# Kernel tuning notes

Measured on AMD Instinct MI355X. Metric: run time of the kernel, lower is better.

The kernel has to match this reference:

```python
import jax, jax.numpy as jnp
import numpy as np

APREC = 8   # activation fractional bits
PPREC = 8   # parameter fractional bits
IWIDTH = 3  # integer width -> clamp to [-2**IWIDTH, 2**IWIDTH - 1]

QMAX = 2.0 ** IWIDTH - 1.0
QMIN = -(2.0 ** IWIDTH)


def quant(v, prec):
    # round to 2**-prec grid (torch.round and jnp.round both round-half-to-even)
    s = 2.0 ** prec
    return jnp.round(v * s) / s


def round_max(v):
    # the relu-chain in the source is exactly a clamp to [QMIN, QMAX]
    return jnp.clip(v, QMIN, QMAX)


def fixed_point_conv(x, w, b):
    """Quantized 'conv': each elementwise product w[j,m,p,q]*x[b,m,k+p,l+q] is
    rounded to the activation grid and clamped BEFORE summation, then bias added.
    x: [B,Cin,H,W], w: [Cout,Cin,K,K], b: [Cout].
    Loop is over the KxK fixed kernel offsets (25), fully vectorized over B/Cout/Cin/space."""
    w = quant(w, PPREC)
    b = quant(b, PPREC)
    K = w.shape[2]
    Ho = x.shape[2] - K + 1
    Wo = x.shape[3] - K + 1
    out = jnp.zeros((x.shape[0], w.shape[0], Ho, Wo), dtype=x.dtype)
    for p in range(K):
        for q in range(K):
            # [B, Cout, Cin, Ho, Wo]
            prod = x[:, None, :, p:p + Ho, q:q + Wo] * w[None, :, :, p, q, None, None]
            prod = round_max(quant(prod, APREC))
            out = out + prod.sum(axis=2)
    return out + b[None, :, None, None]


def fixed_point_fc(x, w, b):
    # x: [B, in], w: [out, in], b: [out]
    w = round_max(quant(w, PPREC))
    b = round_max(quant(b, PPREC))
    x = round_max(quant(x, APREC))
    out = x @ w.T + b[None, :]
    out = round_max(out)
    return quant(out, APREC)


def max_pool2(x):
    return jax.lax.reduce_window(x, -jnp.inf, jax.lax.max,
                                 (1, 1, 2, 2), (1, 1, 2, 2), 'VALID')


def setup_inputs() -> dict:
    key = jax.random.key(0)
    ks = jax.random.split(key, 9)
    B = 2048
    return {
        'x': jax.random.normal(ks[0], (B, 1, 28, 28), jnp.float32),
        'conv1_w': jax.random.normal(ks[1], (10, 1, 5, 5), jnp.float32) * 0.2,
        'conv1_b': jax.random.normal(ks[2], (10,), jnp.float32) * 0.1,
        'conv2_w': jax.random.normal(ks[3], (20, 10, 5, 5), jnp.float32) * 0.1,
        'conv2_b': jax.random.normal(ks[4], (20,), jnp.float32) * 0.1,
        'fc1_w': jax.random.normal(ks[5], (50, 320), jnp.float32) * 0.05,
        'fc1_b': jax.random.normal(ks[6], (50,), jnp.float32) * 0.05,
        'fc2_w': jax.random.normal(ks[7], (10, 50), jnp.float32) * 0.1,
        'fc2_b': jax.random.normal(ks[8], (10,), jnp.float32) * 0.1,
    }


def reference(x, conv1_w, conv1_b, conv2_w, conv2_b, fc1_w, fc1_b, fc2_w, fc2_b):
    x = quant(x, APREC)
    conv1_input = x
    x = fixed_point_conv(x, conv1_w, conv1_b)          # [B,10,24,24]
    x = quant(x, APREC)
    conv1_output = x
    x = jax.nn.relu(max_pool2(x))                      # [B,10,12,12]
    x = quant(x, APREC)
    conv2_input = x
    x = fixed_point_conv(x, conv2_w, conv2_b)          # [B,20,8,8]
    x = quant(x, APREC)
    conv2_output = x
    # Dropout2d / F.dropout are identity in eval mode
    x = jax.nn.relu(max_pool2(x))                      # [B,20,4,4]
    x = x.reshape(-1, 320)
    x = quant(x, APREC)
    fc1_input = x
    x = fixed_point_fc(x, fc1_w, fc1_b)                # [B,50]
    x = quant(x, APREC)
    fc1_output = x
    x = jax.nn.relu(x)
    x = quant(x, APREC)
    fc2_input = x
    x = fixed_point_fc(x, fc2_w, fc2_b)                # [B,10]
    x = quant(x, APREC)
    fc2_output = x
    logp = jax.nn.log_softmax(x, axis=1)
    return (logp, conv1_input, conv1_output, conv2_input, conv2_output,
            fc1_input, fc1_output, fc2_input, fc2_output)
```

## Files before the change

kernel.cpp:

```cpp
#include <hip/hip_runtime.h>
#include <math.h>


#define NB 2048

#define OFF_LOGP   0
#define OFF_C1IN   (OFF_LOGP  + NB*10)
#define OFF_C1OUT  (OFF_C1IN  + NB*784)
#define OFF_C2IN   (OFF_C1OUT + NB*5760)
#define OFF_C2OUT  (OFF_C2IN  + NB*1440)
#define OFF_FC1IN  (OFF_C2OUT + NB*1280)
#define OFF_FC1OUT (OFF_FC1IN + NB*320)
#define OFF_FC2IN  (OFF_FC1OUT+ NB*50)
#define OFF_FC2OUT (OFF_FC2IN + NB*50)

#define MAGIC_F 12582912.0f

#define WS_WT1 0
#define WS_B1  20480
#define WS_WT2 20544
#define WS_B2  21344

__device__ __forceinline__ float clamp8(float v) {
    return __builtin_amdgcn_fmed3f(v, -8.0f, 7.0f);
}

__global__ __launch_bounds__(512, 6)
void k12_convs(const float* __restrict__ x,
               const float* __restrict__ cw1, const float* __restrict__ cb1,
               const float* __restrict__ cw2, const float* __restrict__ cb2,
               const float* __restrict__ fw1, const float* __restrict__ fb1,
               const float* __restrict__ fw2, const float* __restrict__ fb2,
               float* __restrict__ ws,
               float* __restrict__ out)
{
    __shared__ __align__(16) float s_w1[280];
    __shared__ float s_b1[10];
    __shared__ __align__(16) float s_w2[5600];
    __shared__ float s_b2[20];
    __shared__ __align__(16) float s_x[784];
    __shared__ __align__(16) float s_p1[1440];

    const int t   = threadIdx.x;
    const int img = blockIdx.x;

    if (t < 250)                 s_w1[(t/25)*28 + (t%25)] = rintf(cw1[t] * 256.0f);
    else if (t >= 256 && t < 266) s_b1[t - 256] = rintf(cb1[t - 256] * 256.0f);
    else if (t >= 288 && t < 308) s_b2[t - 288] = rintf(cb2[t - 288] * 256.0f);
    for (int idx = t; idx < 5000; idx += 512) {
        int cc = idx / 25, q = idx % 25;
        s_w2[cc * 28 + q] = rintf(cw2[idx] * 256.0f);
    }
    const float* xg = x + (size_t)img * 784;
    float* c1in_g = out + OFF_C1IN + (size_t)img * 784;
    for (int i = t; i < 784; i += 512) {
        float v = rintf(xg[i] * 256.0f) * (1.0f / 256.0f);
        s_x[i] = v;
        c1in_g[i] = v;
    }
    __syncthreads();

    if (t < 480) {
        const int co = t / 48;
        const int r  = t % 48;
        const int i  = r >> 1;
        const int jh = r & 1;

        float wreg[28];
        {
            const float* wb = s_w1 + co * 28;
            #pragma unroll
            for (int k = 0; k < 7; k++) {
                float4 v4 = *(const float4*)(wb + 4 * k);
                wreg[4*k] = v4.x; wreg[4*k+1] = v4.y; wreg[4*k+2] = v4.z; wreg[4*k+3] = v4.w;
            }
        }

        float acc[12];
        #pragma unroll
        for (int j = 0; j < 12; j++) acc[j] = MAGIC_F;

        #pragma unroll
        for (int p = 0; p < 5; p++) {
            float xr[16];
            const float* row = &s_x[(i + p) * 28 + 12 * jh];
            #pragma unroll
            for (int k = 0; k < 4; k++) {
                float4 v4 = *(const float4*)(row + 4 * k);
                xr[4*k] = v4.x; xr[4*k+1] = v4.y; xr[4*k+2] = v4.z; xr[4*k+3] = v4.w;
            }
            #pragma unroll
            for (int q = 0; q < 5; q++) {
                float w = wreg[p * 5 + q];
                #pragma unroll
                for (int j = 0; j < 12; j++)
                    acc[j] = fmaf(xr[q + j], w, acc[j]);
            }
        }
        const float C = MAGIC_F - s_b1[co];
        float v[12];
        #pragma unroll
        for (int j = 0; j < 12; j++) v[j] = (acc[j] - C) * (1.0f / 256.0f);

        float* gdst = out + OFF_C1OUT + (size_t)img * 5760 + co * 576 + i * 24 + 12 * jh;
        #pragma unroll
        for (int k = 0; k < 3; k++) {
            float4 st = { v[4*k], v[4*k+1], v[4*k+2], v[4*k+3] };
            *(float4*)(gdst + 4 * k) = st;
        }

        float m[6];
        #pragma unroll
        for (int j2 = 0; j2 < 6; j2++) m[j2] = fmaxf(v[2*j2], v[2*j2+1]);
        float pm[6];
        #pragma unroll
        for (int j2 = 0; j2 < 6; j2++) pm[j2] = __shfl_xor(m[j2], 2);

        if ((i & 1) == 0) {
            float pr[6];
            #pragma unroll
            for (int j2 = 0; j2 < 6; j2++)
                pr[j2] = fmaxf(fmaxf(m[j2], pm[j2]), 0.0f);
            const int o = co * 144 + (i >> 1) * 12 + 6 * jh;
            float* g = out + OFF_C2IN + (size_t)img * 1440 + o;
            #pragma unroll
            for (int k = 0; k < 3; k++) {
                float2 st = { pr[2*k], pr[2*k+1] };
                *(float2*)(g + 2 * k) = st;
                s_p1[o + 2*k]     = pr[2*k];
                s_p1[o + 2*k + 1] = pr[2*k + 1];
            }
        }
    }
    __syncthreads();

    if (t < 320) {
        const int ch = t & 1;
        const int rc = t >> 1;
        const int co = rc >> 3;
        const int i  = rc & 7;

        float acc[8];
        #pragma unroll
        for (int j = 0; j < 8; j++) acc[j] = MAGIC_F;

        #pragma unroll
        for (int cc = 0; cc < 5; cc++) {
            const int ci = ch * 5 + cc;
            float wreg[28];
            {
                const float* wb = s_w2 + (co * 10 + ci) * 28;
                #pragma unroll
                for (int k = 0; k < 7; k++) {
                    float4 v4 = *(const float4*)(wb + 4 * k);
                    wreg[4*k] = v4.x; wreg[4*k+1] = v4.y; wreg[4*k+2] = v4.z; wreg[4*k+3] = v4.w;
                }
            }
            const float* xb = s_p1 + ci * 144;
            #pragma unroll
            for (int p = 0; p < 5; p++) {
                const float* row = xb + (i + p) * 12;
                float4 a4 = *(const float4*)(row);
                float4 b4 = *(const float4*)(row + 4);
                float4 c4 = *(const float4*)(row + 8);
                float xr[12] = { a4.x, a4.y, a4.z, a4.w, b4.x, b4.y, b4.z, b4.w,
                                 c4.x, c4.y, c4.z, c4.w };
                #pragma unroll
                for (int q = 0; q < 5; q++) {
                    float w = wreg[p * 5 + q];
                    #pragma unroll
                    for (int j = 0; j < 8; j++)
                        acc[j] = fmaf(xr[q + j], w, acc[j]);
                }
            }
        }

        float s[8];
        #pragma unroll
        for (int j = 0; j < 8; j++) s[j] = acc[j] - MAGIC_F;
        #pragma unroll
        for (int j = 0; j < 8; j++) s[j] += __shfl_xor(s[j], 1);

        const float b2 = s_b2[co];
        float v[8];
        #pragma unroll
        for (int j = 0; j < 8; j++) v[j] = (s[j] + b2) * (1.0f / 256.0f);

        float m[4], pm[4];
        #pragma unroll
        for (int c = 0; c < 4; c++) m[c] = fmaxf(v[2*c], v[2*c+1]);
        #pragma unroll
        for (int c = 0; c < 4; c++) pm[c] = __shfl_xor(m[c], 2);

        if (ch == 0) {
            float4 st0 = { v[0], v[1], v[2], v[3] };
            float4 st1 = { v[4], v[5], v[6], v[7] };
            float* cdst = out + OFF_C2OUT + (size_t)img * 1280 + co * 64 + i * 8;
            *(float4*)(cdst)     = st0;
            *(float4*)(cdst + 4) = st1;

            if ((i & 1) == 0) {
                float4 pr = { fmaxf(fmaxf(m[0], pm[0]), 0.0f),
                              fmaxf(fmaxf(m[1], pm[1]), 0.0f),
                              fmaxf(fmaxf(m[2], pm[2]), 0.0f),
                              fmaxf(fmaxf(m[3], pm[3]), 0.0f) };
                *(float4*)(out + OFF_FC1IN + (size_t)img * 320 + co * 16 + (i >> 1) * 4) = pr;
            }
        }
    }

    const int b = blockIdx.x;
    if (b < 50) {
        const float* src = fw1 + b * 320;
        for (int i = t; i < 320; i += 512)
            ws[WS_WT1 + i * 64 + b] = clamp8(rintf(src[i] * 256.0f) * (1.0f / 256.0f));
    } else if (b == 50) {
        for (int idx = t; idx < 320 * 14; idx += 512) {
            int i = idx / 14, j = 50 + idx % 14;
            ws[WS_WT1 + i * 64 + j] = 0.0f;
        }
        for (int idx = t; idx < 800; idx += 512) {
            int k = idx >> 4, j = idx & 15;
            float v = 0.0f;
            if (j < 10) v = clamp8(rintf(fw2[j * 50 + k] * 256.0f) * (1.0f / 256.0f));
            ws[WS_WT2 + idx] = v;
        }
        if (t < 64) ws[WS_B1 + t] = (t < 50) ? clamp8(rintf(fb1[t] * 256.0f) * (1.0f / 256.0f)) : 0.0f;
        if (t < 16) ws[WS_B2 + t] = (t < 10) ? clamp8(rintf(fb2[t] * 256.0f) * (1.0f / 256.0f)) : 0.0f;
    }
}

__global__ __launch_bounds__(256)
void k3_fc(const float* __restrict__ ws, float* __restrict__ out)
{
    __shared__ float s_x[4][320];

    const int t    = threadIdx.x;
    const int wv   = t >> 6;
    const int lane = t & 63;
    const int img  = blockIdx.x * 4 + wv;

    const float* xg = out + OFF_FC1IN + (size_t)img * 320;
    #pragma unroll
    for (int r = 0; r < 5; r++)
        s_x[wv][lane + 64 * r] = clamp8(xg[lane + 64 * r]);
    __syncthreads();

    float acc = ws[WS_B1 + lane];
    #pragma unroll 8
    for (int k = 0; k < 320; k++)
        acc = fmaf(s_x[wv][k], ws[WS_WT1 + k * 64 + lane], acc);
    float o1 = rintf(clamp8(acc) * 256.0f) * (1.0f / 256.0f);
    float r1 = fmaxf(o1, 0.0f);
    if (lane < 50) {
        out[OFF_FC1OUT + (size_t)img * 50 + lane] = o1;
        out[OFF_FC2IN  + (size_t)img * 50 + lane] = r1;
    }
    float yc = clamp8(r1);

    float acc2 = ws[WS_B2 + (lane & 15)];
    #pragma unroll 10
    for (int k = 0; k < 50; k++) {
        float yk = __shfl(yc, k);
        acc2 = fmaf(yk, ws[WS_WT2 + k * 16 + (lane & 15)], acc2);
    }
    float o2 = rintf(clamp8(acc2) * 256.0f) * (1.0f / 256.0f);
    if (lane < 10) out[OFF_FC2OUT + (size_t)img * 10 + lane] = o2;

    float v = (lane < 10) ? o2 : -3.0e38f;
    #pragma unroll
    for (int d = 1; d < 16; d <<= 1)
        v = fmaxf(v, __shfl_xor(v, d, 16));
    float e = (lane < 10) ? expf(o2 - v) : 0.0f;
    #pragma unroll
    for (int d = 1; d < 16; d <<= 1)
        e += __shfl_xor(e, d, 16);
    float lse = v + logf(e);
    if (lane < 10) out[OFF_LOGP + (size_t)img * 10 + lane] = o2 - lse;
}

extern "C" void kernel_launch(void* const* d_in, const int* in_sizes, int n_in,
                              void* d_out, int out_size, void* d_ws, size_t ws_size,
                              hipStream_t stream) {
    const float* x   = (const float*)d_in[0];
    const float* cw1 = (const float*)d_in[1];
    const float* cb1 = (const float*)d_in[2];
    const float* cw2 = (const float*)d_in[3];
    const float* cb2 = (const float*)d_in[4];
    const float* fw1 = (const float*)d_in[5];
    const float* fb1 = (const float*)d_in[6];
    const float* fw2 = (const float*)d_in[7];
    const float* fb2 = (const float*)d_in[8];
    float* o  = (float*)d_out;
    float* ws = (float*)d_ws;

    k12_convs<<<NB, 512, 0, stream>>>(x, cw1, cb1, cw2, cb2, fw1, fb1, fw2, fb2, ws, o);
    k3_fc    <<<NB / 4, 256, 0, stream>>>(ws, o);
}
```

Before: 157.7 us.

## Fuse convs and FC into one wave-per-image kernel with separate weight prep

```diff
diff --git a/kernel.cpp b/kernel.cpp
--- a/kernel.cpp
+++ b/kernel.cpp
@@ -20,125 +20,171 @@
 #define WS_B1  20480
 #define WS_WT2 20544
 #define WS_B2  21344
+#define WS_CW2 21360
+#define WS_CB2 26960
+#define WS_CW1 26980
+#define WS_CB1 27260
 
 __device__ __forceinline__ float clamp8(float v) {
     return __builtin_amdgcn_fmed3f(v, -8.0f, 7.0f);
 }
 
-__global__ __launch_bounds__(512, 6)
-void k12_convs(const float* __restrict__ x,
-               const float* __restrict__ cw1, const float* __restrict__ cb1,
-               const float* __restrict__ cw2, const float* __restrict__ cb2,
-               const float* __restrict__ fw1, const float* __restrict__ fb1,
-               const float* __restrict__ fw2, const float* __restrict__ fb2,
-               float* __restrict__ ws,
-               float* __restrict__ out)
+__global__ __launch_bounds__(256)
+void k0_prep(const float* __restrict__ cw1, const float* __restrict__ cb1,
+             const float* __restrict__ cw2, const float* __restrict__ cb2,
+             const float* __restrict__ fw1, const float* __restrict__ fb1,
+             const float* __restrict__ fw2, const float* __restrict__ fb2,
+             float* __restrict__ ws)
+{
+    const int t = threadIdx.x, b = blockIdx.x;
+    if (b < 50) {
+        const float* src = fw1 + b * 320;
+        for (int i = t; i < 320; i += 256)
+            ws[WS_WT1 + i * 64 + b] = clamp8(rintf(src[i] * 256.0f) * (1.0f / 256.0f));
+    } else if (b == 50) {
+        for (int idx = t; idx < 320 * 14; idx += 256) {
+            int i = idx / 14, j = 50 + idx % 14;
+            ws[WS_WT1 + i * 64 + j] = 0.0f;
+        }
+        for (int idx = t; idx < 800; idx += 256) {
+            int k = idx >> 4, j = idx & 15;
+            ws[WS_WT2 + idx] = (j < 10) ? clamp8(rintf(fw2[j * 50 + k] * 256.0f) * (1.0f / 256.0f)) : 0.0f;
+        }
+        if (t < 64) ws[WS_B1 + t] = (t < 50) ? clamp8(rintf(fb1[t] * 256.0f) * (1.0f / 256.0f)) : 0.0f;
+        if (t < 16) ws[WS_B2 + t] = (t < 10) ? clamp8(rintf(fb2[t] * 256.0f) * (1.0f / 256.0f)) : 0.0f;
+    } else {
+        for (int idx = t; idx < 5600; idx += 256) {
+            int cc = idx / 28, col = idx % 28;
+            ws[WS_CW2 + idx] = (col < 25) ? rintf(cw2[cc * 25 + col] * 256.0f) : 0.0f;
+        }
+        if (t < 20) ws[WS_CB2 + t] = rintf(cb2[t] * 256.0f);
+        for (int idx = t; idx < 280; idx += 256) {
+            int cc = idx / 28, col = idx % 28;
+            ws[WS_CW1 + idx] = (col < 25) ? rintf(cw1[cc * 25 + col] * 256.0f) : 0.0f;
+        }
+        if (t >= 32 && t < 42) ws[WS_CB1 + (t - 32)] = rintf(cb1[t - 32] * 256.0f);
+    }
+}
+
+__global__ __launch_bounds__(256, 2)
+void k12w(const float* __restrict__ x, const float* __restrict__ ws,
+          float* __restrict__ out)
 {
     __shared__ __align__(16) float s_w1[280];
     __shared__ float s_b1[10];
     __shared__ __align__(16) float s_w2[5600];
     __shared__ float s_b2[20];
-    __shared__ __align__(16) float s_x[784];
-    __shared__ __align__(16) float s_p1[1440];
-
-    const int t   = threadIdx.x;
-    const int img = blockIdx.x;
-
-    if (t < 250)                 s_w1[(t/25)*28 + (t%25)] = rintf(cw1[t] * 256.0f);
-    else if (t >= 256 && t < 266) s_b1[t - 256] = rintf(cb1[t - 256] * 256.0f);
-    else if (t >= 288 && t < 308) s_b2[t - 288] = rintf(cb2[t - 288] * 256.0f);
-    for (int idx = t; idx < 5000; idx += 512) {
-        int cc = idx / 25, q = idx % 25;
-        s_w2[cc * 28 + q] = rintf(cw2[idx] * 256.0f);
-    }
-    const float* xg = x + (size_t)img * 784;
-    float* c1in_g = out + OFF_C1IN + (size_t)img * 784;
-    for (int i = t; i < 784; i += 512) {
-        float v = rintf(xg[i] * 256.0f) * (1.0f / 256.0f);
-        s_x[i] = v;
-        c1in_g[i] = v;
+    __shared__ __align__(16) float s_x[4][784];
+    __shared__ __align__(16) float s_p1[4][1440];
+
+    const int t    = threadIdx.x;
+    const int img0 = blockIdx.x * 4;
+
+    {
+        const float4* wsrc = (const float4*)(ws + WS_CW2);
+        float4* wdst = (float4*)s_w2;
+        for (int i = t; i < 1400; i += 256) wdst[i] = wsrc[i];
+        if (t < 70) ((float4*)s_w1)[t] = ((const float4*)(ws + WS_CW1))[t];
+    }
+    if (t >= 70 && t < 80)  s_b1[t - 70] = ws[WS_CB1 + (t - 70)];
+    if (t >= 80 && t < 100) s_b2[t - 80] = ws[WS_CB2 + (t - 80)];
+
+    {
+        const float* xg = x + (size_t)img0 * 784;
+        float* c1in_g = out + OFF_C1IN + (size_t)img0 * 784;
+        float* sxf = &s_x[0][0];
+        for (int i = t; i < 3136; i += 256) {
+            float v = rintf(xg[i] * 256.0f) * (1.0f / 256.0f);
+            sxf[i] = v;
+            c1in_g[i] = v;
+        }
     }
     __syncthreads();
 
-    if (t < 480) {
-        const int co = t / 48;
-        const int r  = t % 48;
-        const int i  = r >> 1;
-        const int jh = r & 1;
-
-        float wreg[28];
-        {
-            const float* wb = s_w1 + co * 28;
-            #pragma unroll
-            for (int k = 0; k < 7; k++) {
-                float4 v4 = *(const float4*)(wb + 4 * k);
-                wreg[4*k] = v4.x; wreg[4*k+1] = v4.y; wreg[4*k+2] = v4.z; wreg[4*k+3] = v4.w;
-            }
-        }
-
-        float acc[12];
-        #pragma unroll
-        for (int j = 0; j < 12; j++) acc[j] = MAGIC_F;
-
+    const int wv  = t >> 6;
+    const int L   = t & 63;
+    const int img = img0 + wv;
+    const float* sx = s_x[wv];
+    float*       sp = s_p1[wv];
+    float*       sf = s_x[wv];
+
+    if (L < 48) {
+        const int i  = L >> 1;
+        const int jh = L & 1;
+
+        float xr[5][16];
         #pragma unroll
         for (int p = 0; p < 5; p++) {
-            float xr[16];
-            const float* row = &s_x[(i + p) * 28 + 12 * jh];
+            const float* row = sx + (i + p) * 28 + 12 * jh;
             #pragma unroll
             for (int k = 0; k < 4; k++) {
                 float4 v4 = *(const float4*)(row + 4 * k);
-                xr[4*k] = v4.x; xr[4*k+1] = v4.y; xr[4*k+2] = v4.z; xr[4*k+3] = v4.w;
-            }
-            #pragma unroll
-            for (int q = 0; q < 5; q++) {
-                float w = wreg[p * 5 + q];
-                #pragma unroll
-                for (int j = 0; j < 12; j++)
-                    acc[j] = fmaf(xr[q + j], w, acc[j]);
-            }
-        }
-        const float C = MAGIC_F - s_b1[co];
-        float v[12];
-        #pragma unroll
-        for (int j = 0; j < 12; j++) v[j] = (acc[j] - C) * (1.0f / 256.0f);
-
-        float* gdst = out + OFF_C1OUT + (size_t)img * 5760 + co * 576 + i * 24 + 12 * jh;
-        #pragma unroll
-        for (int k = 0; k < 3; k++) {
-            float4 st = { v[4*k], v[4*k+1], v[4*k+2], v[4*k+3] };
-            *(float4*)(gdst + 4 * k) = st;
-        }
-
-        float m[6];
-        #pragma unroll
-        for (int j2 = 0; j2 < 6; j2++) m[j2] = fmaxf(v[2*j2], v[2*j2+1]);
-        float pm[6];
-        #pragma unroll
-        for (int j2 = 0; j2 < 6; j2++) pm[j2] = __shfl_xor(m[j2], 2);
-
-        if ((i & 1) == 0) {
-            float pr[6];
-            #pragma unroll
-            for (int j2 = 0; j2 < 6; j2++)
-                pr[j2] = fmaxf(fmaxf(m[j2], pm[j2]), 0.0f);
-            const int o = co * 144 + (i >> 1) * 12 + 6 * jh;
-            float* g = out + OFF_C2IN + (size_t)img * 1440 + o;
+                xr[p][4*k] = v4.x; xr[p][4*k+1] = v4.y; xr[p][4*k+2] = v4.z; xr[p][4*k+3] = v4.w;
+            }
+        }
+
+        for (int co = 0; co < 10; co++) {
+            float wreg[28];
+            {
+                const float* wb = s_w1 + co * 28;
+                #pragma unroll
+                for (int k = 0; k < 7; k++) {
+                    float4 v4 = *(const float4*)(wb + 4 * k);
+                    wreg[4*k] = v4.x; wreg[4*k+1] = v4.y; wreg[4*k+2] = v4.z; wreg[4*k+3] = v4.w;
+                }
+            }
+            float acc[12];
+            #pragma unroll
+            for (int j = 0; j < 12; j++) acc[j] = MAGIC_F;
+            #pragma unroll
+            for (int p = 0; p < 5; p++)
+                #pragma unroll
+                for (int q = 0; q < 5; q++) {
+                    float w = wreg[p * 5 + q];
+                    #pragma unroll
+                    for (int j = 0; j < 12; j++)
+                        acc[j] = fmaf(xr[p][q + j], w, acc[j]);
+                }
+            const float C = MAGIC_F - s_b1[co];
+            float v[12];
+            #pragma unroll
+            for (int j = 0; j < 12; j++) v[j] = (acc[j] - C) * (1.0f / 256.0f);
+
+            float* gdst = out + OFF_C1OUT + (size_t)img * 5760 + co * 576 + i * 24 + 12 * jh;
             #pragma unroll
             for (int k = 0; k < 3; k++) {
-                float2 st = { pr[2*k], pr[2*k+1] };
-                *(float2*)(g + 2 * k) = st;
-                s_p1[o + 2*k]     = pr[2*k];
-                s_p1[o + 2*k + 1] = pr[2*k + 1];
-            }
-        }
-    }
-    __syncthreads();
-
-    if (t < 320) {
-        const int ch = t & 1;
-        const int rc = t >> 1;
-        const int co = rc >> 3;
-        const int i  = rc & 7;
+                float4 st = { v[4*k], v[4*k+1], v[4*k+2], v[4*k+3] };
+                *(float4*)(gdst + 4 * k) = st;
+            }
+
+            float m[6];
+            #pragma unroll
+            for (int j2 = 0; j2 < 6; j2++) m[j2] = fmaxf(v[2*j2], v[2*j2+1]);
+            float pm[6];
+            #pragma unroll
+            for (int j2 = 0; j2 < 6; j2++) pm[j2] = __shfl_xor(m[j2], 2);
+
+            if ((i & 1) == 0) {
+                float pr[6];
+                #pragma unroll
+                for (int j2 = 0; j2 < 6; j2++)
+                    pr[j2] = fmaxf(fmaxf(m[j2], pm[j2]), 0.0f);
+                const int o = co * 144 + (i >> 1) * 12 + 6 * jh;
+                float* g = out + OFF_C2IN + (size_t)img * 1440 + o;
+                #pragma unroll
+                for (int k = 0; k < 3; k++) {
+                    float2 st = { pr[2*k], pr[2*k+1] };
+                    *(float2*)(g + 2 * k) = st;
+                    *(float2*)(sp + o + 2 * k) = st;
+                }
+            }
+        }
+    }
+
+    const int ch = L & 1;
+    const int i2 = (L >> 1) & 7;
+    for (int g = 0; g < 5; g++) {
+        const int co = 4 * g + (L >> 4);
 
         float acc[8];
         #pragma unroll
@@ -156,10 +202,10 @@
                     wreg[4*k] = v4.x; wreg[4*k+1] = v4.y; wreg[4*k+2] = v4.z; wreg[4*k+3] = v4.w;
                 }
             }
-            const float* xb = s_p1 + ci * 144;
+            const float* xb = sp + ci * 144;
             #pragma unroll
             for (int p = 0; p < 5; p++) {
-                const float* row = xb + (i + p) * 12;
+                const float* row = xb + (i2 + p) * 12;
                 float4 a4 = *(const float4*)(row);
                 float4 b4 = *(const float4*)(row + 4);
                 float4 c4 = *(const float4*)(row + 8);
@@ -195,88 +241,54 @@
         if (ch == 0) {
             float4 st0 = { v[0], v[1], v[2], v[3] };
             float4 st1 = { v[4], v[5], v[6], v[7] };
-            float* cdst = out + OFF_C2OUT + (size_t)img * 1280 + co * 64 + i * 8;
+            float* cdst = out + OFF_C2OUT + (size_t)img * 1280 + co * 64 + i2 * 8;
             *(float4*)(cdst)     = st0;
             *(float4*)(cdst + 4) = st1;
 
-            if ((i & 1) == 0) {
+            if ((i2 & 1) == 0) {
                 float4 pr = { fmaxf(fmaxf(m[0], pm[0]), 0.0f),
                               fmaxf(fmaxf(m[1], pm[1]), 0.0f),
                               fmaxf(fmaxf(m[2], pm[2]), 0.0f),
                               fmaxf(fmaxf(m[3], pm[3]), 0.0f) };
-                *(float4*)(out + OFF_FC1IN + (size_t)img * 320 + co * 16 + (i >> 1) * 4) = pr;
-            }
-        }
-    }
-
-    const int b = blockIdx.x;
-    if (b < 50) {
-        const float* src = fw1 + b * 320;
-        for (int i = t; i < 320; i += 512)
-            ws[WS_WT1 + i * 64 + b] = clamp8(rintf(src[i] * 256.0f) * (1.0f / 256.0f));
-    } else if (b == 50) {
-        for (int idx = t; idx < 320 * 14; idx += 512) {
-            int i = idx / 14, j = 50 + idx % 14;
-            ws[WS_WT1 + i * 64 + j] = 0.0f;
-        }
-        for (int idx = t; idx < 800; idx += 512) {
-            int k = idx >> 4, j = idx & 15;
-            float v = 0.0f;
-            if (j < 10) v = clamp8(rintf(fw2[j * 50 + k] * 256.0f) * (1.0f / 256.0f));
-            ws[WS_WT2 + idx] = v;
-        }
-        if (t < 64) ws[WS_B1 + t] = (t < 50) ? clamp8(rintf(fb1[t] * 256.0f) * (1.0f / 256.0f)) : 0.0f;
-        if (t < 16) ws[WS_B2 + t] = (t < 10) ? clamp8(rintf(fb2[t] * 256.0f) * (1.0f / 256.0f)) : 0.0f;
-    }
-}
-
-__global__ __launch_bounds__(256)
-void k3_fc(const float* __restrict__ ws, float* __restrict__ out)
-{
-    __shared__ float s_x[4][320];
-
-    const int t    = threadIdx.x;
-    const int wv   = t >> 6;
-    const int lane = t & 63;
-    const int img  = blockIdx.x * 4 + wv;
-
-    const float* xg = out + OFF_FC1IN + (size_t)img * 320;
-    #pragma unroll
-    for (int r = 0; r < 5; r++)
-        s_x[wv][lane + 64 * r] = clamp8(xg[lane + 64 * r]);
-    __syncthreads();
-
-    float acc = ws[WS_B1 + lane];
+                const int o = co * 16 + (i2 >> 1) * 4;
+                *(float4*)(out + OFF_FC1IN + (size_t)img * 320 + o) = pr;
+                float4 prc = { clamp8(pr.x), clamp8(pr.y), clamp8(pr.z), clamp8(pr.w) };
+                *(float4*)(sf + o) = prc;
+            }
+        }
+    }
+
+    float acc = ws[WS_B1 + L];
     #pragma unroll 8
     for (int k = 0; k < 320; k++)
-        acc = fmaf(s_x[wv][k], ws[WS_WT1 + k * 64 + lane], acc);
+        acc = fmaf(sf[k], ws[WS_WT1 + k * 64 + L], acc);
     float o1 = rintf(clamp8(acc) * 256.0f) * (1.0f / 256.0f);
     float r1 = fmaxf(o1, 0.0f);
-    if (lane < 50) {
-        out[OFF_FC1OUT + (size_t)img * 50 + lane] = o1;
-        out[OFF_FC2IN  + (size_t)img * 50 + lane] = r1;
+    if (L < 50) {
+        out[OFF_FC1OUT + (size_t)img * 50 + L] = o1;
+        out[OFF_FC2IN  + (size_t)img * 50 + L] = r1;
     }
     float yc = clamp8(r1);
 
-    float acc2 = ws[WS_B2 + (lane & 15)];
+    float acc2 = ws[WS_B2 + (L & 15)];
     #pragma unroll 10
     for (int k = 0; k < 50; k++) {
         float yk = __shfl(yc, k);
-        acc2 = fmaf(yk, ws[WS_WT2 + k * 16 + (lane & 15)], acc2);
+        acc2 = fmaf(yk, ws[WS_WT2 + k * 16 + (L & 15)], acc2);
     }
     float o2 = rintf(clamp8(acc2) * 256.0f) * (1.0f / 256.0f);
-    if (lane < 10) out[OFF_FC2OUT + (size_t)img * 10 + lane] = o2;
-
-    float v = (lane < 10) ? o2 : -3.0e38f;
+    if (L < 10) out[OFF_FC2OUT + (size_t)img * 10 + L] = o2;
+
+    float vmx = (L < 10) ? o2 : -3.0e38f;
     #pragma unroll
     for (int d = 1; d < 16; d <<= 1)
-        v = fmaxf(v, __shfl_xor(v, d, 16));
-    float e = (lane < 10) ? expf(o2 - v) : 0.0f;
+        vmx = fmaxf(vmx, __shfl_xor(vmx, d, 16));
+    float e = (L < 10) ? expf(o2 - vmx) : 0.0f;
     #pragma unroll
     for (int d = 1; d < 16; d <<= 1)
         e += __shfl_xor(e, d, 16);
-    float lse = v + logf(e);
-    if (lane < 10) out[OFF_LOGP + (size_t)img * 10 + lane] = o2 - lse;
+    float lse = vmx + logf(e);
+    if (L < 10) out[OFF_LOGP + (size_t)img * 10 + L] = o2 - lse;
 }
 
 extern "C" void kernel_launch(void* const* d_in, const int* in_sizes, int n_in,
@@ -294,6 +306,6 @@
     float* o  = (float*)d_out;
     float* ws = (float*)d_ws;
 
-    k12_convs<<<NB, 512, 0, stream>>>(x, cw1, cb1, cw2, cb2, fw1, fb1, fw2, fb2, ws, o);
-    k3_fc    <<<NB / 4, 256, 0, stream>>>(ws, o);
+    k0_prep<<<52, 256, 0, stream>>>(cw1, cb1, cw2, cb2, fw1, fb1, fw2, fb2, ws);
+    k12w   <<<NB / 4, 256, 0, stream>>>(x, ws, o);
 }
```

New measurement: 309.6 us. 1.96x slower.
